# Optimization experiments

Measured on AMD Instinct MI355X. Metric: run time of the kernel, lower is better.

The kernel has to match this reference:

```python
import jax, jax.numpy as jnp
import numpy as np

PRIME = 2147483647  # 2^31 - 1, MinHash modulus
GAMMA = 0.3
NUM_HEADS = 8


def minhash_sketch(ids, a, b):
    # ids: (B, L, S) int64 atom ids; a,b: (K,) hash coefficients
    # h[b,l,s,k] = (a[k]*id + b[k]) mod PRIME ; signature = min over the set axis S
    h = (ids[..., None] * a + b) % PRIME          # (B, L, S, K)
    return h.min(axis=2)                          # (B, L, K)


def jaccard_from_signatures(sig_q, sig_k):
    # sig_q: (B, Lq, K), sig_k: (B, Lk, K) -> (B, Lq, Lk) fraction of matching slots.
    # Scan over the K hash slots to avoid materializing a (B,Lq,Lk,K) tensor.
    B, Lq, K = sig_q.shape
    Lk = sig_k.shape[1]

    def step(acc, cols):
        qc, kc = cols                              # (B,Lq), (B,Lk)
        return acc + (qc[:, :, None] == kc[:, None, :]).astype(jnp.float32), None

    init = jnp.zeros((B, Lq, Lk), jnp.float32)
    xs = (jnp.moveaxis(sig_q, -1, 0), jnp.moveaxis(sig_k, -1, 0))
    acc, _ = jax.lax.scan(step, init, xs)
    return acc / K


def symdiff_from_jaccard(jacc, size_q, size_k):
    # |A ∩ B| = J/(1+J) * (|A|+|B|)  =>  |A Δ B| = (|A|+|B|) * (1-J)/(1+J)
    tot = size_q[:, :, None] + size_k[:, None, :]   # (B, Lq, Lk)
    return tot * (1.0 - jacc) / (1.0 + jacc)


def setup_inputs() -> dict:
    key = jax.random.key(0)
    ks = jax.random.split(key, 12)
    B, Lq, Lk, E, S, K, V = 4, 1024, 1024, 512, 8, 128, 32000
    w = lambda k: (jax.random.normal(k, (E, E), jnp.float32) * 0.02)
    return {
        "query": jax.random.normal(ks[0], (B, Lq, E), jnp.float32),
        "key": jax.random.normal(ks[1], (B, Lk, E), jnp.float32),
        "value": jax.random.normal(ks[2], (B, Lk, E), jnp.float32),
        "token_sets_q": jax.random.randint(ks[3], (B, Lq, S), 0, V).astype(jnp.int64),
        "token_sets_k": jax.random.randint(ks[4], (B, Lk, S), 0, V).astype(jnp.int64),
        "hash_a": jax.random.randint(ks[5], (K,), 1, PRIME - 1).astype(jnp.int64),
        "hash_b": jax.random.randint(ks[6], (K,), 0, PRIME - 1).astype(jnp.int64),
        "Wq": w(ks[7]), "bq": jnp.zeros((E,), jnp.float32),
        "Wk": w(ks[8]), "bk": jnp.zeros((E,), jnp.float32),
        "Wv": w(ks[9]), "bv": jnp.zeros((E,), jnp.float32),
        "Wo": w(ks[10]), "bo": jnp.zeros((E,), jnp.float32),
    }


def reference(query, key, value, token_sets_q, token_sets_k, hash_a, hash_b,
              Wq, bq, Wk, bk, Wv, bv, Wo, bo):
    B, Lq, E = query.shape
    Lk = key.shape[1]
    H = NUM_HEADS
    d = E // H

    # in-projections (torch Linear: x @ W^T + b); q,k are computed but the
    # attention scores come solely from the token-set kernel (gating disabled)
    q = query @ Wq.T + bq
    k = key @ Wk.T + bk
    v = (value @ Wv.T + bv).reshape(B, Lk, H, d).transpose(0, 2, 1, 3)  # (B,H,Lk,d)

    # MinHash sketches of per-token atom sets -> estimated Jaccard -> Δ-RBF score
    sig_q = minhash_sketch(token_sets_q, hash_a, hash_b)   # (B,Lq,K)
    sig_k = minhash_sketch(token_sets_k, hash_a, hash_b)   # (B,Lk,K)
    jacc = jaccard_from_signatures(sig_q, sig_k)           # (B,Lq,Lk)

    S = token_sets_q.shape[-1]
    size_q = jnp.full((B, Lq), S, jnp.float32)             # uniform CSR offsets -> |set| = S
    size_k = jnp.full((B, Lk), S, jnp.float32)
    delta = symdiff_from_jaccard(jacc, size_q, size_k)
    scores = jnp.exp(-GAMMA * delta)                       # (B,Lq,Lk), shared by all heads

    attn = jax.nn.softmax(scores, axis=-1)                 # no masks, no causal, dropout=0
    ctx = jnp.einsum('bqk,bhkd->bqhd', attn, v).reshape(B, Lq, E)
    return ctx @ Wo.T + bo
```

## Files before the change

kernel.cpp:

```cpp
#include <hip/hip_runtime.h>
#include <hip/hip_bf16.h>
#include <stdint.h>

#define PRIME 2147483647u
#define GAMMA 0.3f
#define K_HASH 128
#define S_SET 8
#define NB 4
#define LQ 1024
#define LK 1024
#define EDIM 512

typedef unsigned short ushort_t;
typedef __attribute__((ext_vector_type(8))) short short8;
typedef __attribute__((ext_vector_type(4))) float f32x4;

static __device__ __forceinline__ unsigned short f2bf(float f) {
    unsigned u = __builtin_bit_cast(unsigned, f);
    u += 0x7FFFu + ((u >> 16) & 1u);
    return (unsigned short)(u >> 16);
}

static __device__ __forceinline__ void glds16(const void* g, void* l) {
    __builtin_amdgcn_global_load_lds(
        (const __attribute__((address_space(1))) unsigned int*)g,
        (__attribute__((address_space(3))) unsigned int*)l, 16, 0, 0);
}

#define SWZ(r) ((((r) >> 2) & 3) ^ ((r) & 3))

static __device__ __forceinline__ unsigned nm2(unsigned acc, unsigned a,
                                               unsigned b, unsigned ones) {
    unsigned x = a ^ b, t;
    asm("v_pk_min_u16 %0, %1, %2" : "=v"(t) : "v"(x), "v"(ones));
    return acc + t;
}
static __device__ __forceinline__ unsigned nm8(unsigned acc, int4 q, int4 k,
                                               unsigned ones) {
    acc = nm2(acc, (unsigned)q.x, (unsigned)k.x, ones);
    acc = nm2(acc, (unsigned)q.y, (unsigned)k.y, ones);
    acc = nm2(acc, (unsigned)q.z, (unsigned)k.z, ones);
    acc = nm2(acc, (unsigned)q.w, (unsigned)k.w, ones);
    return acc;
}

#define EPI_NONE     0
#define EPI_DIVBIAS  1

template<int OUTF32, int MODE>
static __device__ void gemm64(
        const ushort_t* __restrict__ A, const ushort_t* __restrict__ B,
        void* __restrict__ C,
        const float* __restrict__ bias, const float* __restrict__ scale,
        int lda, int ldb, int ldc, int Kd, int m0, int n0,
        ushort_t* AsBase, ushort_t* BsBase, int tid) {
    ushort_t (*As)[64 * 32] = (ushort_t (*)[64 * 32])AsBase;
    ushort_t (*Bs)[64 * 32] = (ushort_t (*)[64 * 32])BsBase;
    int w = tid >> 6, lane = tid & 63;
    int wm = (w & 1) * 32, wn = (w >> 1) * 32;
    int mrow = lane & 15, kg = lane >> 4;

    int r = tid >> 2, c = (tid & 3) ^ SWZ(r);
    const ushort_t* pa = A + (size_t)(m0 + r) * lda + c * 8;
    const ushort_t* pb = B + (size_t)(n0 + r) * ldb + c * 8;

    int aoff[2], boff[2];
    #pragma unroll
    for (int s = 0; s < 2; s++) {
        int Ra = wm + s * 16 + mrow;
        aoff[s] = Ra * 32 + (kg ^ SWZ(Ra)) * 8;
        int Rb = wn + s * 16 + mrow;
        boff[s] = Rb * 32 + (kg ^ SWZ(Rb)) * 8;
    }

    f32x4 acc[2][2] = {};
    int nK = Kd >> 5;
    glds16(pa, &As[0][tid * 8]);
    glds16(pb, &Bs[0][tid * 8]);
    for (int i = 0; i < nK; i++) {
        __syncthreads();
        int cur = i & 1, nxt = cur ^ 1;
        if (i + 1 < nK) {
            int k0 = (i + 1) << 5;
            glds16(pa + k0, &As[nxt][tid * 8]);
            glds16(pb + k0, &Bs[nxt][tid * 8]);
        }
        short8 af[2], bh[2];
        #pragma unroll
        for (int s = 0; s < 2; s++) {
            af[s] = *(const short8*)&As[cur][aoff[s]];
            bh[s] = *(const short8*)&Bs[cur][boff[s]];
        }
        #pragma unroll
        for (int ii = 0; ii < 2; ii++)
            #pragma unroll
            for (int jj = 0; jj < 2; jj++)
                acc[ii][jj] = __builtin_amdgcn_mfma_f32_16x16x32_bf16(
                                  af[ii], bh[jj], acc[ii][jj], 0, 0, 0);
    }

    int col = lane & 15, rbase = (lane >> 4) * 4;
    #pragma unroll
    for (int ii = 0; ii < 2; ii++) {
        #pragma unroll
        for (int jj = 0; jj < 2; jj++) {
            #pragma unroll
            for (int rr = 0; rr < 4; rr++) {
                int gm = m0 + wm + ii * 16 + rbase + rr;
                int gn = n0 + wn + jj * 16 + col;
                float v = acc[ii][jj][rr];
                if (MODE == EPI_DIVBIAS) v = v / scale[gm] + bias[gn];
                size_t cix = (size_t)gm * ldc + gn;
                if (OUTF32) ((float*)C)[cix] = v;
                else        ((ushort_t*)C)[cix] = f2bf(v);
            }
        }
    }
}

#define PREP_WO   128
#define PREP_TV   512
#define PREP_TW   64
#define PREP_SIG  1024
#define PREP_B2   2
#define PREP_BLOCKS (PREP_WO + PREP_TV + PREP_TW + PREP_SIG + PREP_B2)

union PrepSmem {
    ushort_t Ts[64][66];
    float bvs[512];
};

static __device__ void tconvert(const float* __restrict__ src,
                                ushort_t* __restrict__ dst,
                                int R, int C, int r0, int c0, int tid,
                                ushort_t (*Ts)[66]) {
    int rr = tid >> 2, c4 = (tid & 3) * 16;
    const float* s = src + (size_t)(r0 + rr) * C + c0 + c4;
    float4 a = *(const float4*)(s + 0), b = *(const float4*)(s + 4);
    float4 cc = *(const float4*)(s + 8), d = *(const float4*)(s + 12);
    ushort_t* tr = &Ts[rr][c4];
    tr[0]=f2bf(a.x);  tr[1]=f2bf(a.y);  tr[2]=f2bf(a.z);  tr[3]=f2bf(a.w);
    tr[4]=f2bf(b.x);  tr[5]=f2bf(b.y);  tr[6]=f2bf(b.z);  tr[7]=f2bf(b.w);
    tr[8]=f2bf(cc.x); tr[9]=f2bf(cc.y); tr[10]=f2bf(cc.z); tr[11]=f2bf(cc.w);
    tr[12]=f2bf(d.x); tr[13]=f2bf(d.y); tr[14]=f2bf(d.z); tr[15]=f2bf(d.w);
    __syncthreads();
    int er = tid >> 3, bc = (tid & 7) * 8;
    #pragma unroll
    for (int it = 0; it < 2; it++) {
        int e = er + it * 32;
        ushort_t tmp[8];
        #pragma unroll
        for (int i = 0; i < 8; i++) tmp[i] = Ts[bc + i][e];
        *(short8*)&dst[(size_t)(c0 + e) * R + r0 + bc] = *(const short8*)tmp;
    }
}

__global__ __launch_bounds__(256) void prep_kernel(
        const float* __restrict__ value, const float* __restrict__ wv,
        const float* __restrict__ wo,
        const float* __restrict__ bv, const float* __restrict__ bo,
        const int* __restrict__ tsq, const int* __restrict__ tsk,
        const int* __restrict__ ha, const int* __restrict__ hb,
        ushort_t* __restrict__ VbT, ushort_t* __restrict__ WvT,
        ushort_t* __restrict__ Wob,
        ushort_t* __restrict__ sigq, ushort_t* __restrict__ sigk,
        float* __restrict__ rs, float* __restrict__ bias2) {
    __shared__ PrepSmem sm;
    int blk = blockIdx.x, tid = threadIdx.x;
    if (blk < 16) rs[blk * 256 + tid] = 0.f;
    if (blk < PREP_WO) {
        size_t i = ((size_t)blk * 256 + tid) * 8;
        float4 a = *(const float4*)(wo + i), b = *(const float4*)(wo + i + 4);
        ushort4 o0, o1;
        o0.x=f2bf(a.x); o0.y=f2bf(a.y); o0.z=f2bf(a.z); o0.w=f2bf(a.w);
        o1.x=f2bf(b.x); o1.y=f2bf(b.y); o1.z=f2bf(b.z); o1.w=f2bf(b.w);
        *(ushort4*)(Wob + i)     = o0;
        *(ushort4*)(Wob + i + 4) = o1;
        return;
    }
    if (blk < PREP_WO + PREP_TV) {
        int t = blk - PREP_WO;
        tconvert(value, VbT, NB * LK, EDIM, (t & 63) * 64, (t >> 6) * 64, tid, sm.Ts);
        return;
    }
    if (blk < PREP_WO + PREP_TV + PREP_TW) {
        int t = blk - PREP_WO - PREP_TV;
        tconvert(wv, WvT, EDIM, EDIM, (t & 7) * 64, (t >> 3) * 64, tid, sm.Ts);
        return;
    }
    if (blk < PREP_WO + PREP_TV + PREP_TW + PREP_SIG) {
        int sb = blk - PREP_WO - PREP_TV - PREP_TW;
        int k = tid & 127, half = tid >> 7;
        unsigned long long a  = (unsigned)ha[k];
        unsigned long long bb = (unsigned)hb[k];
        #pragma unroll
        for (int p = 0; p < 4; p++) {
            int row = sb * 8 + p * 2 + half;
            const int* ts = (row < NB * LQ) ? tsq : tsk;
            ushort_t* sig = (row < NB * LQ) ? sigq : sigk;
            int idx = row & (NB * LQ - 1);
            unsigned mn = 0xFFFFFFFFu;
            #pragma unroll
            for (int s = 0; s < S_SET; s++) {
                unsigned long long x =
                    a * (unsigned long long)(unsigned)ts[idx * S_SET + s] + bb;
                x = (x & PRIME) + (x >> 31);
                x = (x & PRIME) + (x >> 31);
                unsigned r = (unsigned)x;
                if (r >= PRIME) r -= PRIME;
                mn = (r < mn) ? r : mn;
            }
            sig[idx * K_HASH + k] = (ushort_t)mn;
        }
        return;
    }
    int sb2 = blk - (PREP_BLOCKS - PREP_B2);
    sm.bvs[tid] = bv[tid];
    sm.bvs[256 + tid] = bv[256 + tid];
    __syncthreads();
    int n = sb2 * 256 + tid;
    float acc = bo[n];
    #pragma unroll 8
    for (int e = 0; e < EDIM; e++) acc += wo[(size_t)n * EDIM + e] * sm.bvs[e];
    bias2[n] = acc;
}

union JacwSmem {
    struct {
        int Qs[4][64 * 16];
        int Ks[4][64 * 17];
        float lut[K_HASH + 1];
    } jac;
    struct {
        ushort_t As[2][64 * 32];
        ushort_t Bs[2][64 * 32];
    } g;
};

__global__ __launch_bounds__(256) void jacw_kernel(
        const ushort_t* __restrict__ sigq, const ushort_t* __restrict__ sigk,
        ushort_t* __restrict__ P, float* __restrict__ rs,
        const ushort_t* __restrict__ Wob, const ushort_t* __restrict__ WvT,
        ushort_t* __restrict__ W2) {
    __shared__ JacwSmem sm;
    int blk = blockIdx.x, tid = threadIdx.x;
    if (blk >= 1024) {
        int t = blk - 1024;
        gemm64<0, EPI_NONE>(Wob, WvT, W2, nullptr, nullptr,
                            EDIM, EDIM, EDIM, EDIM,
                            (t >> 3) * 64, (t & 7) * 64,
                            sm.g.As[0], sm.g.Bs[0], tid);
        return;
    }
    if (tid <= K_HASH) {
        float r = (float)(K_HASH - tid) / (float)(K_HASH + tid);
        sm.jac.lut[tid] = expf(expf(-GAMMA * (2.0f * S_SET) * r));
    }
    int b = blk >> 8;
    int q0 = ((blk >> 4) & 15) * 64, j0 = (blk & 15) * 64;
    const int4* gq = (const int4*)(sigq + ((size_t)b * LQ + q0) * K_HASH);
    const int4* gk = (const int4*)(sigk + ((size_t)b * LK + j0) * K_HASH);
    int r0 = tid >> 2, g0 = tid & 3;
    #pragma unroll
    for (int ch = 0; ch < 4; ch++) {
        *(int4*)&sm.jac.Qs[ch][r0 * 16 + ((g0 + (r0 >> 3)) & 3) * 4]
            = gq[r0 * 16 + ch * 4 + g0];
        *(int4*)&sm.jac.Ks[ch][r0 * 17 + ((g0 + (r0 >> 5)) & 3) * 4]
            = gk[r0 * 16 + ch * 4 + g0];
    }
    __syncthreads();
    int tx = tid & 15, ty = tid >> 4;
    unsigned ones = 0x00010001u;
    unsigned acc[4][4] = {};
    #pragma unroll 1
    for (int ch = 0; ch < 4; ch++) {
        #pragma unroll
        for (int cc = 0; cc < 4; cc++) {
            int qo = ((cc + (ty >> 1)) & 3) * 4;
            int ko = ((cc + (tx >> 3)) & 3) * 4;
            int4 qv[4], kv[4];
            #pragma unroll
            for (int i = 0; i < 4; i++)
                qv[i] = *(const int4*)&sm.jac.Qs[ch][(ty * 4 + i) * 16 + qo];
            #pragma unroll
            for (int j = 0; j < 4; j++)
                kv[j] = *(const int4*)&sm.jac.Ks[ch][(tx * 4 + j) * 17 + ko];
            #pragma unroll
            for (int i = 0; i < 4; i++)
                #pragma unroll
                for (int j = 0; j < 4; j++)
                    acc[i][j] = nm8(acc[i][j], qv[i], kv[j], ones);
        }
    }
    ushort_t* Pb = P + (size_t)b * LQ * LK;
    float fsum[4];
    #pragma unroll
    for (int i = 0; i < 4; i++) {
        ushort4 o;
        unsigned n0_ = (acc[i][0] & 0xFFFFu) + (acc[i][0] >> 16);
        unsigned n1_ = (acc[i][1] & 0xFFFFu) + (acc[i][1] >> 16);
        unsigned n2_ = (acc[i][2] & 0xFFFFu) + (acc[i][2] >> 16);
        unsigned n3_ = (acc[i][3] & 0xFFFFu) + (acc[i][3] >> 16);
        float p0 = sm.jac.lut[K_HASH - n0_], p1 = sm.jac.lut[K_HASH - n1_];
        float p2 = sm.jac.lut[K_HASH - n2_], p3 = sm.jac.lut[K_HASH - n3_];
        fsum[i] = (p0 + p1) + (p2 + p3);
        o.x = f2bf(p0); o.y = f2bf(p1); o.z = f2bf(p2); o.w = f2bf(p3);
        int row = q0 + ty * 4 + i;
        *(ushort4*)&Pb[(size_t)row * LK + j0 + tx * 4] = o;
    }
    __syncthreads();
    float* fs = (float*)&sm.jac.Qs[0][0];
    #pragma unroll
    for (int i = 0; i < 4; i++) fs[(ty * 4 + i) * 16 + tx] = fsum[i];
    __syncthreads();
    if (tid < 64) {
        float s = 0.f;
        #pragma unroll
        for (int t = 0; t < 16; t++) s += fs[tid * 16 + t];
        atomicAdd(&rs[(size_t)b * LQ + q0 + tid], s);
    }
}

__global__ __launch_bounds__(256) void gemm_ctx2_kernel(
        const ushort_t* __restrict__ P, const ushort_t* __restrict__ VbT,
        ushort_t* __restrict__ ctx2) {
    __shared__ ushort_t As[2][64 * 32], Bs[2][64 * 32];
    int z = blockIdx.z;
    gemm64<0, EPI_NONE>(P + (size_t)z * LQ * LK, VbT + (size_t)z * LK,
                        ctx2 + (size_t)z * LQ * EDIM, nullptr, nullptr,
                        LK, NB * LK, EDIM, LK,
                        blockIdx.y * 64, blockIdx.x * 64,
                        As[0], Bs[0], threadIdx.x);
}

__global__ __launch_bounds__(256) void gemm_out_kernel(
        const ushort_t* __restrict__ ctx2, const ushort_t* __restrict__ W2,
        float* __restrict__ out, const float* __restrict__ bias2,
        const float* __restrict__ rs) {
    __shared__ ushort_t As[2][64 * 32], Bs[2][64 * 32];
    gemm64<1, EPI_DIVBIAS>(ctx2, W2, out, bias2, rs,
                           EDIM, EDIM, EDIM, EDIM,
                           blockIdx.y * 64, blockIdx.x * 64,
                           As[0], Bs[0], threadIdx.x);
}

extern "C" void kernel_launch(void* const* d_in, const int* in_sizes, int n_in,
                              void* d_out, int out_size, void* d_ws, size_t ws_size,
                              hipStream_t stream) {
    const float* value = (const float*)d_in[2];
    const int* tsq = (const int*)d_in[3];
    const int* tsk = (const int*)d_in[4];
    const int* ha  = (const int*)d_in[5];
    const int* hb  = (const int*)d_in[6];
    const float* Wv = (const float*)d_in[11];
    const float* bv = (const float*)d_in[12];
    const float* Wo = (const float*)d_in[13];
    const float* bo = (const float*)d_in[14];
    float* out = (float*)d_out;

    char* ws = (char*)d_ws;
    ushort_t* sigq  = (ushort_t*)(ws);
    ushort_t* sigk  = (ushort_t*)(ws + (1ull << 20));
    float*    rs    = (float*)(ws + (2ull << 20));
    float*    bias2 = (float*)(ws + (2ull << 20) + (64 << 10));
    ushort_t* P     = (ushort_t*)(ws + (4ull << 20));
    ushort_t* VbT   = (ushort_t*)(ws + (12ull << 20));
    ushort_t* ctx2  = (ushort_t*)(ws + (16ull << 20));
    ushort_t* Wob   = (ushort_t*)(ws + (20ull << 20));
    ushort_t* WvT   = (ushort_t*)(ws + (20ull << 20) + (512 << 10));
    ushort_t* W2    = (ushort_t*)(ws + (21ull << 20));

    prep_kernel<<<PREP_BLOCKS, 256, 0, stream>>>(
        value, Wv, Wo, bv, bo, tsq, tsk, ha, hb,
        VbT, WvT, Wob, sigq, sigk, rs, bias2);

    jacw_kernel<<<1024 + 64, 256, 0, stream>>>(sigq, sigk, P, rs, Wob, WvT, W2);

    gemm_ctx2_kernel<<<dim3(EDIM / 64, LQ / 64, NB), 256, 0, stream>>>(P, VbT, ctx2);

    gemm_out_kernel<<<dim3(EDIM / 64, NB * LQ / 64, 1), 256, 0, stream>>>(
        ctx2, W2, out, bias2, rs);
}
```

Measured before the change: 168.0 us.

## Enlarge Jaccard tile to 128x64 with XOR-swizzled LDS and remap ctx GEMM grid

The Jaccard/probability kernel now computes 128 query rows by 64 key rows per block, so each thread holds an 8x4 accumulator tile. The whole 128-slot signature sits in LDS with a padded stride and an XOR swizzle, which halves the block count and raises K-signature reuse per LDS load. The ctx GEMM moves to a 1D grid whose ordering keeps blocks that share the same output column tile adjacent, aiming at better L2 reuse of VbT. In exchange, registers and LDS per block grow, which may lower occupancy, and there are fewer blocks to fill the CUs.

```diff
diff --git a/kernel.cpp b/kernel.cpp
--- a/kernel.cpp
+++ b/kernel.cpp
@@ -227,8 +227,8 @@
 
 union JacwSmem {
     struct {
-        int Qs[4][64 * 16];
-        int Ks[4][64 * 17];
+        int Qs[128 * 72];
+        int Ks[64 * 72];
         float lut[K_HASH + 1];
     } jac;
     struct {
@@ -244,8 +244,8 @@
         ushort_t* __restrict__ W2) {
     __shared__ JacwSmem sm;
     int blk = blockIdx.x, tid = threadIdx.x;
-    if (blk >= 1024) {
-        int t = blk - 1024;
+    if (blk >= 512) {
+        int t = blk - 512;
         gemm64<0, EPI_NONE>(Wob, WvT, W2, nullptr, nullptr,
                             EDIM, EDIM, EDIM, EDIM,
                             (t >> 3) * 64, (t & 7) * 64,
@@ -256,46 +256,47 @@
         float r = (float)(K_HASH - tid) / (float)(K_HASH + tid);
         sm.jac.lut[tid] = expf(expf(-GAMMA * (2.0f * S_SET) * r));
     }
-    int b = blk >> 8;
-    int q0 = ((blk >> 4) & 15) * 64, j0 = (blk & 15) * 64;
+    int b = blk >> 7;
+    int q0 = ((blk >> 4) & 7) * 128, j0 = (blk & 15) * 64;
     const int4* gq = (const int4*)(sigq + ((size_t)b * LQ + q0) * K_HASH);
     const int4* gk = (const int4*)(sigk + ((size_t)b * LK + j0) * K_HASH);
     int r0 = tid >> 2, g0 = tid & 3;
+    int r1 = 64 + r0;
     #pragma unroll
     for (int ch = 0; ch < 4; ch++) {
-        *(int4*)&sm.jac.Qs[ch][r0 * 16 + ((g0 + (r0 >> 3)) & 3) * 4]
-            = gq[r0 * 16 + ch * 4 + g0];
-        *(int4*)&sm.jac.Ks[ch][r0 * 17 + ((g0 + (r0 >> 5)) & 3) * 4]
-            = gk[r0 * 16 + ch * 4 + g0];
+        int g = ch * 4 + g0;
+        *(int4*)&sm.jac.Qs[r0 * 72 + ((g ^ (r0 >> 3)) & 15) * 4] = gq[r0 * 16 + g];
+        *(int4*)&sm.jac.Qs[r1 * 72 + ((g ^ (r1 >> 3)) & 15) * 4] = gq[r1 * 16 + g];
+        *(int4*)&sm.jac.Ks[r0 * 72 + ((g ^ (r0 >> 2)) & 15) * 4] = gk[r0 * 16 + g];
     }
     __syncthreads();
     int tx = tid & 15, ty = tid >> 4;
     unsigned ones = 0x00010001u;
-    unsigned acc[4][4] = {};
+    unsigned acc[8][4] = {};
     #pragma unroll 1
     for (int ch = 0; ch < 4; ch++) {
         #pragma unroll
         for (int cc = 0; cc < 4; cc++) {
-            int qo = ((cc + (ty >> 1)) & 3) * 4;
-            int ko = ((cc + (tx >> 3)) & 3) * 4;
-            int4 qv[4], kv[4];
-            #pragma unroll
-            for (int i = 0; i < 4; i++)
-                qv[i] = *(const int4*)&sm.jac.Qs[ch][(ty * 4 + i) * 16 + qo];
+            int g = ch * 4 + cc;
+            int qx = ((g ^ ty) & 15) * 4, kx = ((g ^ tx) & 15) * 4;
+            int4 qv[8], kv[4];
+            #pragma unroll
+            for (int i = 0; i < 8; i++)
+                qv[i] = *(const int4*)&sm.jac.Qs[(ty * 8 + i) * 72 + qx];
             #pragma unroll
             for (int j = 0; j < 4; j++)
-                kv[j] = *(const int4*)&sm.jac.Ks[ch][(tx * 4 + j) * 17 + ko];
-            #pragma unroll
-            for (int i = 0; i < 4; i++)
+                kv[j] = *(const int4*)&sm.jac.Ks[(tx * 4 + j) * 72 + kx];
+            #pragma unroll
+            for (int i = 0; i < 8; i++)
                 #pragma unroll
                 for (int j = 0; j < 4; j++)
                     acc[i][j] = nm8(acc[i][j], qv[i], kv[j], ones);
         }
     }
     ushort_t* Pb = P + (size_t)b * LQ * LK;
-    float fsum[4];
-    #pragma unroll
-    for (int i = 0; i < 4; i++) {
+    float fsum[8];
+    #pragma unroll
+    for (int i = 0; i < 8; i++) {
         ushort4 o;
         unsigned n0_ = (acc[i][0] & 0xFFFFu) + (acc[i][0] >> 16);
         unsigned n1_ = (acc[i][1] & 0xFFFFu) + (acc[i][1] >> 16);
@@ -305,15 +306,15 @@
         float p2 = sm.jac.lut[K_HASH - n2_], p3 = sm.jac.lut[K_HASH - n3_];
         fsum[i] = (p0 + p1) + (p2 + p3);
         o.x = f2bf(p0); o.y = f2bf(p1); o.z = f2bf(p2); o.w = f2bf(p3);
-        int row = q0 + ty * 4 + i;
+        int row = q0 + ty * 8 + i;
         *(ushort4*)&Pb[(size_t)row * LK + j0 + tx * 4] = o;
     }
     __syncthreads();
-    float* fs = (float*)&sm.jac.Qs[0][0];
-    #pragma unroll
-    for (int i = 0; i < 4; i++) fs[(ty * 4 + i) * 16 + tx] = fsum[i];
-    __syncthreads();
-    if (tid < 64) {
+    float* fs = (float*)&sm.jac.Qs[0];
+    #pragma unroll
+    for (int i = 0; i < 8; i++) fs[(ty * 8 + i) * 16 + tx] = fsum[i];
+    __syncthreads();
+    if (tid < 128) {
         float s = 0.f;
         #pragma unroll
         for (int t = 0; t < 16; t++) s += fs[tid * 16 + t];
@@ -325,12 +326,15 @@
         const ushort_t* __restrict__ P, const ushort_t* __restrict__ VbT,
         ushort_t* __restrict__ ctx2) {
     __shared__ ushort_t As[2][64 * 32], Bs[2][64 * 32];
-    int z = blockIdx.z;
+    int id = blockIdx.x;
+    int n0 = (id >> 6) * 64;
+    int rem = id & 63;
+    int z = rem >> 4;
+    int q0 = (rem & 15) * 64;
     gemm64<0, EPI_NONE>(P + (size_t)z * LQ * LK, VbT + (size_t)z * LK,
                         ctx2 + (size_t)z * LQ * EDIM, nullptr, nullptr,
                         LK, NB * LK, EDIM, LK,
-                        blockIdx.y * 64, blockIdx.x * 64,
-                        As[0], Bs[0], threadIdx.x);
+                        q0, n0, As[0], Bs[0], threadIdx.x);
 }
 
 __global__ __launch_bounds__(256) void gemm_out_kernel(
@@ -374,9 +378,9 @@
         value, Wv, Wo, bv, bo, tsq, tsk, ha, hb,
         VbT, WvT, Wob, sigq, sigk, rs, bias2);
 
-    jacw_kernel<<<1024 + 64, 256, 0, stream>>>(sigq, sigk, P, rs, Wob, WvT, W2);
-
-    gemm_ctx2_kernel<<<dim3(EDIM / 64, LQ / 64, NB), 256, 0, stream>>>(P, VbT, ctx2);
+    jacw_kernel<<<512 + 64, 256, 0, stream>>>(sigq, sigk, P, rs, Wob, WvT, W2);
+
+    gemm_ctx2_kernel<<<512, 256, 0, stream>>>(P, VbT, ctx2);
 
     gemm_out_kernel<<<dim3(EDIM / 64, NB * LQ / 64, 1), 256, 0, stream>>>(
         ctx2, W2, out, bias2, rs);
```

New measurement: 168.9 us. Within noise of the previous version (+0.5%).
